# Performance work log

Measured on AMD Instinct MI355X. Metric: run time of the kernel, lower is better.

The kernel has to match this reference:

```python
import jax, jax.numpy as jnp
import numpy as np

B, S, HIDDEN, N_HEADS = 1, 2048, 2048, 16
HEAD_DIM = HIDDEN // N_HEADS  # 128


def setup_inputs() -> dict:
    key = jax.random.key(0)
    ks = jax.random.split(key, 7)
    w = 0.02  # init scale for projection weights
    return {
        "x_self": jax.random.normal(ks[0], (B, S, HIDDEN), jnp.float32),
        "x_cross": jax.random.normal(ks[1], (B, S, HIDDEN), jnp.float32),
        "mask": jnp.zeros((B, 1, S, S), jnp.float32),
        "Wq": jax.random.normal(ks[2], (HIDDEN, HIDDEN), jnp.float32) * w,
        "Wk": jax.random.normal(ks[3], (HIDDEN, HIDDEN), jnp.float32) * w,
        "Wv": jax.random.normal(ks[4], (HIDDEN, HIDDEN), jnp.float32) * w,
        "Wo": jax.random.normal(ks[5], (HIDDEN, HIDDEN), jnp.float32) * w,
    }


def reference(x_self, x_cross, mask, Wq, Wk, Wv, Wo):
    bf16 = jnp.bfloat16
    b = x_self.shape[0]
    scale = HEAD_DIM ** -0.5

    def split_heads(x):  # [b, s, hidden] -> [b, h, s, d]
        return x.reshape(b, -1, N_HEADS, HEAD_DIM).transpose(0, 2, 1, 3)

    # projections run in bf16 (weights cast to bf16 in the original)
    q_self = split_heads((x_self.astype(bf16) @ Wq.astype(bf16).T))
    q_cross = split_heads((x_cross.astype(bf16) @ Wq.astype(bf16).T))
    # k/v for both self and cross blocks come from x_self with identical weights
    k = split_heads((x_self.astype(bf16) @ Wk.astype(bf16).T))
    v = split_heads((x_self.astype(bf16) @ Wv.astype(bf16).T))

    def attn_block(qh):
        # fp32 upcast for QK^T + softmax, then bf16 cast for AV (dropout p=0 -> identity)
        w = jnp.einsum('bhqd,bhkd->bhqk', qh.astype(jnp.float32), k.astype(jnp.float32)) * scale
        w = w + mask
        w = jax.nn.softmax(w, axis=-1).astype(bf16)
        return jnp.einsum('bhqk,bhkd->bhqd', w, v.astype(bf16))  # [b, h, s, d] bf16

    out_self = attn_block(q_self)
    out_cross = attn_block(q_cross)
    out = jnp.concatenate([out_self, out_cross], axis=1)          # [b, 2h, s, d]
    out_flat = out.transpose(0, 2, 1, 3).reshape(b, -1, HIDDEN)   # [b, 2s, hidden]
    Wo_bf = Wo.astype(bf16)
    out_final = 0.5 * (out_flat @ Wo_bf.T + out_flat @ Wo_bf.T)
    return out_final.astype(jnp.float32)
```

## Files before the change

### kernel.cpp

```cpp
#include <hip/hip_runtime.h>
#include <hip/hip_bf16.h>
#include <stdint.h>

#define S 2048
#define HID 2048
#define NH 16
#define HD 128

typedef short short8 __attribute__((ext_vector_type(8)));
typedef float f32x4 __attribute__((ext_vector_type(4)));
typedef float f32x16 __attribute__((ext_vector_type(16)));
typedef uint32_t u32;
typedef u32 u32x4 __attribute__((ext_vector_type(4)));

__device__ __forceinline__ ushort f2bf(float x) {
  uint32_t u = __builtin_bit_cast(uint32_t, x);
  if ((u & 0x7fffffffu) > 0x7f800000u) return (ushort)((u >> 16) | 0x40);
  uint32_t r = u + 0x7fffu + ((u >> 16) & 1u);
  return (ushort)(r >> 16);
}
__device__ __forceinline__ float bf2f(ushort u) {
  union { uint32_t i; float f; } c; c.i = ((uint32_t)u) << 16; return c.f;
}

__device__ __forceinline__ void glds16(const ushort* g, ushort* l) {
  __builtin_amdgcn_global_load_lds((const __attribute__((address_space(1))) uint32_t*)g,
                                   (__attribute__((address_space(3))) uint32_t*)l, 16, 0, 0);
}

__device__ __forceinline__ void mfma16(f32x4& d, short8 a, short8 b) {
  asm volatile("v_mfma_f32_16x16x32_bf16 %0, %1, %2, %0" : "+v"(d) : "v"(a), "v"(b));
}
__device__ __forceinline__ void mfma32(f32x16& d, short8 a, short8 b) {
  asm volatile("v_mfma_f32_32x32x16_bf16 %0, %1, %2, %0" : "+v"(d) : "v"(a), "v"(b));
}
__device__ __forceinline__ f32x16 mfma32_z(short8 a, short8 b) {
  f32x16 d;
  asm volatile("v_mfma_f32_32x32x16_bf16 %0, %1, %2, 0" : "=v"(d) : "v"(a), "v"(b));
  return d;
}
#define MFMA_FENCE() do {                              \
    asm volatile("s_nop 7\n\ts_nop 7\n\ts_nop 7");     \
    __builtin_amdgcn_sched_barrier(0);                 \
  } while (0)
#define RAW_BARRIER() asm volatile("s_barrier" ::: "memory")
#define SCHED_FENCE() __builtin_amdgcn_sched_barrier(0)
#define MAX3(a, b, c) fmaxf(fmaxf((a), (b)), (c))
__device__ __forceinline__ void plswap(u32& a, u32& b) {
  asm volatile("v_permlane32_swap_b32 %0, %1" : "+v"(a), "+v"(b));
}
__device__ __forceinline__ u32 cvtpk(float lo, float hi) {
  u32 r; asm volatile("v_cvt_pk_bf16_f32 %0, %1, %2" : "=v"(r) : "v"(lo), "v"(hi)); return r;
}

struct CastArgs { const float* s[6]; ushort* d[6]; };
__global__ __launch_bounds__(256) void cast6_k(CastArgs a) {
  const float* in = a.s[blockIdx.y];
  ushort* out = a.d[blockIdx.y];
  int i = blockIdx.x * 256 + threadIdx.x;
  float4 v = ((const float4*)in)[i];
  ushort4 o;
  o.x = f2bf(v.x); o.y = f2bf(v.y); o.z = f2bf(v.z); o.w = f2bf(v.w);
  ((ushort4*)out)[i] = o;
}

template <int OUTF32, int NSPLIT>
__device__ __forceinline__ void gemm256_body(const ushort* __restrict__ A,
                                             const ushort* __restrict__ B,
                                             void* __restrict__ C, int N, int K,
                                             long m0, long n0,
                                             ushort* ldsA, ushort* ldsB) {
  const int tid = threadIdx.x, lane = tid & 63, wid = tid >> 6;
  const int g = lane >> 4, c = lane & 15;
  const int wr = wid >> 2, wc = wid & 3;
  const int srow = lane >> 3, sslot = lane & 7;

  f32x4 acc[8][4] = {};

#define GSTAGE256(BO, K0) do {                                                \
    _Pragma("unroll")                                                         \
    for (int i_ = 0; i_ < 4; ++i_) {                                          \
      int ii = wid * 4 + i_;                \
      int rt = ii * 8 + srow;                                                 \
      int col = ((sslot ^ (rt & 7)) << 3) + (K0);                             \
      glds16(A + (m0 + rt) * (long)K + col, ldsA + (BO) * 16384 + ii * 512);  \
      glds16(B + (n0 + rt) * (long)K + col, ldsB + (BO) * 16384 + ii * 512);  \
    } } while (0)

  GSTAGE256(0, 0);

#pragma clang loop unroll(disable)
  for (int k0 = 0; k0 < K; k0 += 64) {
    const int bo = (k0 >> 6) & 1;
    GSTAGE256(bo ^ 1, (k0 + 64 < K) ? (k0 + 64) : 0);
    SCHED_FENCE();
    asm volatile("s_waitcnt vmcnt(8)");
    SCHED_FENCE();
    RAW_BARRIER();
    const ushort* la = ldsA + bo * 16384;
    const ushort* lb = ldsB + bo * 16384;
#pragma unroll
    for (int kk = 0; kk < 2; ++kk) {
      short8 af[8], bfr[4];
#pragma unroll
      for (int m = 0; m < 8; ++m) {
        int row = wr * 128 + m * 16 + c;
        af[m] = *(const short8*)(la + row * 64 + (((kk * 4 + g) ^ (row & 7)) << 3));
      }
#pragma unroll
      for (int n = 0; n < 4; ++n) {
        int row = wc * 64 + n * 16 + c;
        bfr[n] = *(const short8*)(lb + row * 64 + (((kk * 4 + g) ^ (row & 7)) << 3));
      }
#pragma unroll
      for (int m = 0; m < 8; ++m)
#pragma unroll
        for (int n = 0; n < 4; ++n) mfma16(acc[m][n], af[m], bfr[n]);
    }
    RAW_BARRIER();
  }
#undef GSTAGE256
  MFMA_FENCE();
#pragma unroll
  for (int m = 0; m < 8; ++m) {
#pragma unroll
    for (int r = 0; r < 4; ++r) {
      long grow = m0 + wr * 128 + m * 16 + g * 4 + r;
#pragma unroll
      for (int n = 0; n < 4; ++n) {
        long gcol = n0 + wc * 64 + n * 16 + c;
        long idx;
        if (NSPLIT) idx = ((gcol >> 11) << 22) + (grow << 11) + (gcol & 2047);
        else        idx = grow * N + gcol;
        float v = acc[m][n][r];
        if (OUTF32) ((float*)C)[idx] = bf2f(f2bf(v));
        else        ((ushort*)C)[idx] = f2bf(v);
      }
    }
  }
}

__global__ __launch_bounds__(512)
void gemm_qkv256_k(const ushort* __restrict__ xs, const ushort* __restrict__ Wq,
                   ushort* __restrict__ q, const ushort* __restrict__ Wkv,
                   ushort* __restrict__ kv) {
  __shared__ __align__(16) ushort ldsA[2 * 256 * 64];
  __shared__ __align__(16) ushort ldsB[2 * 256 * 64];
  const int bid = blockIdx.x;
  if (bid < 128) {
    gemm256_body<0, 0>(xs, Wq, q, 2048, 2048,
                       (long)(bid >> 3) * 256, (long)(bid & 7) * 256, ldsA, ldsB);
  } else {
    const int b2 = bid - 128;
    gemm256_body<0, 1>(xs, Wkv, kv, 4096, 2048,
                       (long)(b2 >> 4) * 256, (long)(b2 & 15) * 256, ldsA, ldsB);
  }
}

template <int OUTF32, int NSPLIT>
__global__ __launch_bounds__(256)
void gemm_bt_k(const ushort* __restrict__ A, const ushort* __restrict__ B,
               void* __restrict__ C, int M, int N, int K) {
  __shared__ __align__(16) ushort ldsA[128 * 64];
  __shared__ __align__(16) ushort ldsB[128 * 64];
  const int tid = threadIdx.x, lane = tid & 63, wid = tid >> 6;
  const int g = lane >> 4, c = lane & 15;
  const int wr = wid >> 1, wc = wid & 1;
  const long m0 = (long)blockIdx.y * 128, n0 = (long)blockIdx.x * 128;
  const int srow = lane >> 3, sslot = lane & 7;

  f32x4 acc[4][4] = {};

  for (int k0 = 0; k0 < K; k0 += 64) {
#pragma unroll
    for (int i = 0; i < 4; ++i) {
      int ii = wid * 4 + i;
      int rt = ii * 8 + srow;
      int col = ((sslot ^ (rt & 7)) << 3) + k0;
      glds16(A + (m0 + rt) * (long)K + col, ldsA + ii * 512);
      glds16(B + (n0 + rt) * (long)K + col, ldsB + ii * 512);
    }
    __syncthreads();
#pragma unroll
    for (int kk = 0; kk < 2; ++kk) {
      short8 af[4], bfr[4];
#pragma unroll
      for (int m = 0; m < 4; ++m) {
        int row = wr * 64 + m * 16 + c;
        af[m] = *(const short8*)(ldsA + row * 64 + (((kk * 4 + g) ^ (row & 7)) << 3));
      }
#pragma unroll
      for (int n = 0; n < 4; ++n) {
        int row = wc * 64 + n * 16 + c;
        bfr[n] = *(const short8*)(ldsB + row * 64 + (((kk * 4 + g) ^ (row & 7)) << 3));
      }
#pragma unroll
      for (int m = 0; m < 4; ++m)
#pragma unroll
        for (int n = 0; n < 4; ++n) mfma16(acc[m][n], af[m], bfr[n]);
    }
    __syncthreads();
  }
  MFMA_FENCE();
#pragma unroll
  for (int m = 0; m < 4; ++m) {
#pragma unroll
    for (int r = 0; r < 4; ++r) {
      long grow = m0 + wr * 64 + m * 16 + g * 4 + r;
#pragma unroll
      for (int n = 0; n < 4; ++n) {
        long gcol = n0 + wc * 64 + n * 16 + c;
        long idx;
        if (NSPLIT) idx = ((gcol >> 11) << 22) + (grow << 11) + (gcol & 2047);
        else        idx = grow * N + gcol;
        float v = acc[m][n][r];
        if (OUTF32) ((float*)C)[idx] = bf2f(f2bf(v));
        else        ((ushort*)C)[idx] = f2bf(v);
      }
    }
  }
}

__global__ __launch_bounds__(256)
void transpose_bf16_k(const ushort* __restrict__ in, ushort* __restrict__ out) {
  __shared__ __align__(16) ushort t[64][72];
  const int tid = threadIdx.x;
  const long bx = (long)blockIdx.x * 64;
  const long by = (long)blockIdx.y * 64;
#pragma unroll
  for (int i = 0; i < 2; ++i) {
    int row = (tid >> 3) + i * 32;
    int col = (tid & 7) * 8;
    *(short8*)(&t[row][col]) = *(const short8*)(in + (by + row) * 2048 + bx + col);
  }
  __syncthreads();
#pragma unroll
  for (int i = 0; i < 2; ++i) {
    int orow = (tid >> 3) + i * 32;
    int ocol = (tid & 7) * 8;
    short8 v;
#pragma unroll
    for (int j = 0; j < 8; ++j) v[j] = (short)t[ocol + j][orow];
    *(short8*)(out + (bx + orow) * 2048 + by + ocol) = v;
  }
}

__global__ __launch_bounds__(256)
void maskQ_k(const float* __restrict__ in, ushort* __restrict__ out) {
  __shared__ ushort t[64][72];
  const int tid = threadIdx.x;
  const long q0 = (long)blockIdx.y * 64;
  const long k0 = (long)blockIdx.x * 64;
#pragma unroll
  for (int i = 0; i < 4; ++i) {
    int row = i * 16 + (tid >> 4);
    int col = (tid & 15) * 4;
    float4 v = *(const float4*)(in + (q0 + row) * S + k0 + col);
    t[col + 0][row] = f2bf(v.x);
    t[col + 1][row] = f2bf(v.y);
    t[col + 2][row] = f2bf(v.z);
    t[col + 3][row] = f2bf(v.w);
  }
  __syncthreads();
#pragma unroll
  for (int i = 0; i < 4; ++i) {
    int r4 = i * 4 + (tid >> 6);
    int q = tid & 63;
    ushort4 o;
    o.x = t[r4 * 4 + 0][q];
    o.y = t[r4 * 4 + 1][q];
    o.z = t[r4 * 4 + 2][q];
    o.w = t[r4 * 4 + 3][q];
    *(ushort4*)(out + ((k0 >> 2) + r4) * (S * 4) + (q0 + q) * 4) = o;
  }
}

__global__ __launch_bounds__(256)
void attn7_k(const ushort* __restrict__ Qself, const ushort* __restrict__ Qcross,
             const ushort* __restrict__ Kp, const ushort* __restrict__ Vt,
             const ushort* __restrict__ maskQ, ushort* __restrict__ outf) {
  __shared__ __align__(16) ushort ldsK[2 * 64 * 128];
  __shared__ __align__(16) ushort ldsV[2 * 128 * 64];
  const int tid = threadIdx.x, lane = tid & 63, wid = tid >> 6;
  const int c31 = lane & 31, hi = lane >> 5;

  const int b = blockIdx.x;
  const int xcd = b & 7, j = b >> 3;
  const int h = xcd + 8 * (j & 1);
  const int blk = (j >> 1) & 1;
  const int qt = j >> 2;

  const ushort* Qp = blk ? Qcross : Qself;
  const int qbase = qt * 128 + wid * 32;
  const long qme = qbase + c31;

  short8 qf[8];
#pragma unroll
  for (int ks = 0; ks < 8; ++ks)
    qf[ks] = *(const short8*)(Qp + qme * HID + h * HD + ks * 16 + hi * 8);

  f32x16 o[4] = {};
  float m_r = -__builtin_inff(), l_r = 0.f;

  const float SC  = 0.08838834764831845f;
  const float L2E = 1.4426950408889634f;
  const float THR = 5.545177444479562f;

  const int kRow4 = lane >> 4, kSlot = lane & 15;
  const int vRow8 = lane >> 3, vSlot = lane & 7;
  const ushort* mqp = maskQ + qme * 4 + hi * (S * 4);

#define STAGE(BO, KV0) do {                                                       \
    _Pragma("unroll")                                                             \
    for (int i_ = 0; i_ < 4; ++i_) {                                              \
      int seg = i_ * 4 + wid;                                                     \
      int rk = seg * 4 + kRow4;                                                   \
      glds16(Kp + (long)((KV0) + rk) * HID + h * HD + ((kSlot ^ (rk & 15)) << 3), \
             ldsK + (BO) * 8192 + seg * 512);                                     \
      int rv = seg * 8 + vRow8;                                                   \
      glds16(Vt + (long)(h * HD + rv) * S + (KV0) + ((vSlot ^ (rv & 7)) << 3),    \
             ldsV + (BO) * 8192 + seg * 512);                                     \
    }                                                                             \
  } while (0)

  STAGE(0, 0);

#pragma clang loop unroll(disable)
  for (int t = 0; t < 32; ++t) {
    const int bo = t & 1;
    const ushort* kb = ldsK + bo * 8192;
    const ushort* vb = ldsV + bo * 8192;

    ushort4 mq4[8];
#pragma unroll
    for (int jj = 0; jj < 8; ++jj)
      mq4[jj] = *(const ushort4*)(mqp + ((jj & 3) * 2 + (jj >> 2) * 8) * (S * 4));
    SCHED_FENCE();
    STAGE(bo ^ 1, ((t + 1) & 31) * 64);
    SCHED_FENCE();
    asm volatile("s_waitcnt vmcnt(16)");
    SCHED_FENCE();
    RAW_BARRIER();

    f32x16 s0, s1;
    __builtin_amdgcn_s_setprio(1);
    {
      const int r0 = c31, r1 = 32 + c31;
      short8 kf0 = *(const short8*)(kb + r0 * 128 + ((hi ^ (r0 & 15)) << 3));
      short8 kf1 = *(const short8*)(kb + r1 * 128 + ((hi ^ (r1 & 15)) << 3));
      s0 = mfma32_z(kf0, qf[0]);
      s1 = mfma32_z(kf1, qf[0]);
    }
#pragma unroll
    for (int ks = 1; ks < 8; ++ks) {
      int r0 = c31, r1 = 32 + c31;
      short8 kf0 = *(const short8*)(kb + r0 * 128 + (((ks * 2 + hi) ^ (r0 & 15)) << 3));
      short8 kf1 = *(const short8*)(kb + r1 * 128 + (((ks * 2 + hi) ^ (r1 & 15)) << 3));
      mfma32(s0, kf0, qf[ks]);
      mfma32(s1, kf1, qf[ks]);
    }
    __builtin_amdgcn_s_setprio(0);
    MFMA_FENCE();

#pragma unroll
    for (int r = 0; r < 16; ++r) {
      s0[r] = __builtin_fmaf(s0[r], SC, bf2f(mq4[r >> 2][r & 3]));
      s1[r] = __builtin_fmaf(s1[r], SC, bf2f(mq4[4 + (r >> 2)][r & 3]));
    }

    float a0 = MAX3(s0[0], s0[1], s0[2]);
    float a1 = MAX3(s0[3], s0[4], s0[5]);
    float a2 = MAX3(s0[6], s0[7], s0[8]);
    float a3 = MAX3(s0[9], s0[10], s0[11]);
    float a4 = MAX3(s0[12], s0[13], s0[14]);
    float a5 = MAX3(s0[15], s1[0], s1[1]);
    float a6 = MAX3(s1[2], s1[3], s1[4]);
    float a7 = MAX3(s1[5], s1[6], s1[7]);
    float a8 = MAX3(s1[8], s1[9], s1[10]);
    float a9 = MAX3(s1[11], s1[12], s1[13]);
    float a10 = fmaxf(s1[14], s1[15]);
    float b0 = MAX3(a0, a1, a2);
    float b1 = MAX3(a3, a4, a5);
    float b2 = MAX3(a6, a7, a8);
    float b3 = fmaxf(a9, a10);
    float pm = MAX3(b0, b1, fmaxf(b2, b3));
    float pmax = fmaxf(pm, __shfl_xor(pm, 32));

    if (!__all(pmax <= m_r + THR)) {
      float mnew = fmaxf(m_r, pmax);
      float alpha = __builtin_amdgcn_exp2f((m_r - mnew) * L2E);
      m_r = mnew;
      l_r *= alpha;
#pragma unroll
      for (int r = 0; r < 16; ++r) {
        float alf = __shfl(alpha, (r & 3) + 8 * (r >> 2) + 4 * hi);
#pragma unroll
        for (int dt = 0; dt < 4; ++dt) o[dt][r] *= alf;
      }
    }

    const float nm = -m_r * L2E;
#pragma unroll
    for (int r = 0; r < 16; ++r) {
      s0[r] = __builtin_amdgcn_exp2f(__builtin_fmaf(s0[r], L2E, nm));
      s1[r] = __builtin_amdgcn_exp2f(__builtin_fmaf(s1[r], L2E, nm));
    }
    float sm[16];
#pragma unroll
    for (int r = 0; r < 16; ++r) sm[r] = s0[r] + s1[r];
#pragma unroll
    for (int st = 8; st >= 1; st >>= 1)
#pragma unroll
      for (int i = 0; i < 8; ++i)
        if (i < st) sm[i] += sm[i + st];
    l_r += sm[0] + __shfl_xor(sm[0], 32);

    short8 pa[4];
#pragma unroll
    for (int kk = 0; kk < 4; ++kk) {
      const f32x16& sv = (kk < 2) ? s0 : s1;
      const int bq = (kk & 1) * 8;
      u32 x0 = cvtpk(sv[bq + 0], sv[bq + 1]);
      u32 x1 = cvtpk(sv[bq + 2], sv[bq + 3]);
      u32 y0 = cvtpk(sv[bq + 4], sv[bq + 5]);
      u32 y1 = cvtpk(sv[bq + 6], sv[bq + 7]);
      plswap(x0, y0);
      plswap(x1, y1);
      u32x4 tt; tt[0] = x0; tt[1] = x1; tt[2] = y0; tt[3] = y1;
      pa[kk] = __builtin_bit_cast(short8, tt);
    }
    asm volatile("s_nop 1");
    SCHED_FENCE();

    __builtin_amdgcn_s_setprio(1);
#pragma unroll
    for (int kk = 0; kk < 4; ++kk) {
#pragma unroll
      for (int dt = 0; dt < 4; ++dt) {
        int row = dt * 32 + c31;
        short8 vf = *(const short8*)(vb + row * 64 + (((kk * 2 + hi) ^ (row & 7)) << 3));
        mfma32(o[dt], pa[kk], vf);
      }
    }
    __builtin_amdgcn_s_setprio(0);

    RAW_BARRIER();
    mqp += 16 * (S * 4);
  }
#undef STAGE

  MFMA_FENCE();
#pragma unroll
  for (int r = 0; r < 16; ++r) {
    int qr = (r & 3) + 8 * (r >> 2) + 4 * hi;
    float linv = 1.0f / __shfl(l_r, qr);
    long orow = 2L * (qbase + qr) + blk;
#pragma unroll
    for (int dt = 0; dt < 4; ++dt)
      outf[orow * HID + h * HD + dt * 32 + c31] = f2bf(o[dt][r] * linv);
  }
}

extern "C" void kernel_launch(void* const* d_in, const int* in_sizes, int n_in,
                              void* d_out, int out_size, void* d_ws, size_t ws_size,
                              hipStream_t stream) {
  (void)in_sizes; (void)n_in; (void)out_size; (void)ws_size;
  const float* x_self  = (const float*)d_in[0];
  const float* x_cross = (const float*)d_in[1];
  const float* mask    = (const float*)d_in[2];
  const float* Wq      = (const float*)d_in[3];
  const float* Wk      = (const float*)d_in[4];
  const float* Wv      = (const float*)d_in[5];
  const float* Wo      = (const float*)d_in[6];

  uint8_t* w = (uint8_t*)d_ws;
  const size_t MB8 = (size_t)S * HID * sizeof(ushort);
  ushort* xs_bf   = (ushort*)(w + 0 * MB8);
  ushort* xc_bf   = (ushort*)(w + 1 * MB8);
  ushort* Wq_bf   = (ushort*)(w + 2 * MB8);
  ushort* Wk_bf   = (ushort*)(w + 3 * MB8);
  ushort* Wv_bf   = (ushort*)(w + 4 * MB8);
  ushort* Wo_bf   = (ushort*)(w + 5 * MB8);
  ushort* q_self  = (ushort*)(w + 6 * MB8);
  ushort* q_cross = (ushort*)(w + 7 * MB8);
  ushort* k_      = (ushort*)(w + 8 * MB8);
  ushort* v_      = (ushort*)(w + 9 * MB8);
  ushort* vt       = xs_bf;
  ushort* out_flat = Wq_bf;
  ushort* maskQ    = v_;

  CastArgs ca;
  ca.s[0] = x_self;  ca.d[0] = xs_bf;
  ca.s[1] = x_cross; ca.d[1] = xc_bf;
  ca.s[2] = Wq;      ca.d[2] = Wq_bf;
  ca.s[3] = Wk;      ca.d[3] = Wk_bf;
  ca.s[4] = Wv;      ca.d[4] = Wv_bf;
  ca.s[5] = Wo;      ca.d[5] = Wo_bf;
  cast6_k<<<dim3(4096, 6), 256, 0, stream>>>(ca);

  gemm_qkv256_k<<<dim3(256), 512, 0, stream>>>(xs_bf, Wq_bf, q_self, Wk_bf, k_);

  transpose_bf16_k<<<dim3(32, 32), 256, 0, stream>>>(v_, vt);
  maskQ_k<<<dim3(32, 32), 256, 0, stream>>>(mask, maskQ);

  attn7_k<<<dim3(512), 256, 0, stream>>>(q_self, q_cross, k_, vt, maskQ, out_flat);

  gemm_bt_k<1, 0><<<dim3(16, 32), 256, 0, stream>>>(out_flat, Wo_bf, d_out, 4096, 2048, 2048);
}
```

Baseline: 237.1 us.

## Skip mask loads when mask is all zero; double-buffer 256x128 output GEMM

The mask conversion kernel now ORs a device flag when it sees any nonzero mask value. The attention kernel reads that flag and, when the mask is all zero, runs a loop variant that skips the per-tile mask loads and adds, with a tighter vmcnt wait. The output projection GEMM is replaced by a 512-thread, 256x128-tile kernel with double-buffered LDS staging, so global loads overlap the MFMA work. This adds a memset, an atomic and a duplicated loop body, and the flag is stored in the reused x_cross workspace.

New measurement: 236.2 us. About the same (-0.4%).

```diff
diff --git a/kernel.cpp b/kernel.cpp
--- a/kernel.cpp
+++ b/kernel.cpp
@@ -80,7 +80,7 @@
 #define GSTAGE256(BO, K0) do {                                                \
     _Pragma("unroll")                                                         \
     for (int i_ = 0; i_ < 4; ++i_) {                                          \
-      int ii = wid * 4 + i_;                \
+      int ii = wid * 4 + i_;                                                  \
       int rt = ii * 8 + srow;                                                 \
       int col = ((sslot ^ (rt & 7)) << 3) + (K0);                             \
       glds16(A + (m0 + rt) * (long)K + col, ldsA + (BO) * 16384 + ii * 512);  \
@@ -157,50 +157,70 @@
   }
 }
 
-template <int OUTF32, int NSPLIT>
-__global__ __launch_bounds__(256)
-void gemm_bt_k(const ushort* __restrict__ A, const ushort* __restrict__ B,
-               void* __restrict__ C, int M, int N, int K) {
-  __shared__ __align__(16) ushort ldsA[128 * 64];
-  __shared__ __align__(16) ushort ldsB[128 * 64];
+__global__ __launch_bounds__(512)
+void gemm_out256_k(const ushort* __restrict__ A, const ushort* __restrict__ B,
+                   float* __restrict__ C) {
+  __shared__ __align__(16) ushort ldsA[2 * 256 * 64];
+  __shared__ __align__(16) ushort ldsB[2 * 128 * 64];
   const int tid = threadIdx.x, lane = tid & 63, wid = tid >> 6;
   const int g = lane >> 4, c = lane & 15;
   const int wr = wid >> 1, wc = wid & 1;
-  const long m0 = (long)blockIdx.y * 128, n0 = (long)blockIdx.x * 128;
+  const long m0 = (long)(blockIdx.x >> 4) * 256;
+  const long n0 = (long)(blockIdx.x & 15) * 128;
   const int srow = lane >> 3, sslot = lane & 7;
+  const int K = 2048;
 
   f32x4 acc[4][4] = {};
 
+#define OSTAGE(BO, K0) do {                                                   \
+    _Pragma("unroll")                                                         \
+    for (int i_ = 0; i_ < 4; ++i_) {                                          \
+      int ii = wid * 4 + i_;                       \
+      int rt = ii * 8 + srow;                                                 \
+      int col = ((sslot ^ (rt & 7)) << 3) + (K0);                             \
+      glds16(A + (m0 + rt) * (long)K + col, ldsA + (BO) * 16384 + ii * 512);  \
+    }                                                                         \
+    _Pragma("unroll")                                                         \
+    for (int i_ = 0; i_ < 2; ++i_) {                                          \
+      int ii = wid * 2 + i_;                       \
+      int rt = ii * 8 + srow;                                                 \
+      int col = ((sslot ^ (rt & 7)) << 3) + (K0);                             \
+      glds16(B + (n0 + rt) * (long)K + col, ldsB + (BO) * 8192 + ii * 512);   \
+    } } while (0)
+
+  OSTAGE(0, 0);
+
+#pragma clang loop unroll(disable)
   for (int k0 = 0; k0 < K; k0 += 64) {
-#pragma unroll
-    for (int i = 0; i < 4; ++i) {
-      int ii = wid * 4 + i;
-      int rt = ii * 8 + srow;
-      int col = ((sslot ^ (rt & 7)) << 3) + k0;
-      glds16(A + (m0 + rt) * (long)K + col, ldsA + ii * 512);
-      glds16(B + (n0 + rt) * (long)K + col, ldsB + ii * 512);
-    }
-    __syncthreads();
+    const int bo = (k0 >> 6) & 1;
+    OSTAGE(bo ^ 1, (k0 + 64 < K) ? (k0 + 64) : 0);
+    SCHED_FENCE();
+    asm volatile("s_waitcnt vmcnt(6)");
+    SCHED_FENCE();
+    RAW_BARRIER();
+    const ushort* la = ldsA + bo * 16384;
+    const ushort* lb = ldsB + bo * 8192;
 #pragma unroll
     for (int kk = 0; kk < 2; ++kk) {
       short8 af[4], bfr[4];
 #pragma unroll
       for (int m = 0; m < 4; ++m) {
         int row = wr * 64 + m * 16 + c;
-        af[m] = *(const short8*)(ldsA + row * 64 + (((kk * 4 + g) ^ (row & 7)) << 3));
+        af[m] = *(const short8*)(la + row * 64 + (((kk * 4 + g) ^ (row & 7)) << 3));
       }
 #pragma unroll
       for (int n = 0; n < 4; ++n) {
         int row = wc * 64 + n * 16 + c;
-        bfr[n] = *(const short8*)(ldsB + row * 64 + (((kk * 4 + g) ^ (row & 7)) << 3));
+        bfr[n] = *(const short8*)(lb + row * 64 + (((kk * 4 + g) ^ (row & 7)) << 3));
       }
 #pragma unroll
       for (int m = 0; m < 4; ++m)
 #pragma unroll
         for (int n = 0; n < 4; ++n) mfma16(acc[m][n], af[m], bfr[n]);
     }
-    __syncthreads();
-  }
+    RAW_BARRIER();
+  }
+#undef OSTAGE
   MFMA_FENCE();
 #pragma unroll
   for (int m = 0; m < 4; ++m) {
@@ -210,12 +230,7 @@
 #pragma unroll
       for (int n = 0; n < 4; ++n) {
         long gcol = n0 + wc * 64 + n * 16 + c;
-        long idx;
-        if (NSPLIT) idx = ((gcol >> 11) << 22) + (grow << 11) + (gcol & 2047);
-        else        idx = grow * N + gcol;
-        float v = acc[m][n][r];
-        if (OUTF32) ((float*)C)[idx] = bf2f(f2bf(v));
-        else        ((ushort*)C)[idx] = f2bf(v);
+        C[grow * 2048 + gcol] = bf2f(f2bf(acc[m][n][r]));
       }
     }
   }
@@ -246,21 +261,25 @@
 }
 
 __global__ __launch_bounds__(256)
-void maskQ_k(const float* __restrict__ in, ushort* __restrict__ out) {
+void maskQ_k(const float* __restrict__ in, ushort* __restrict__ out,
+             u32* __restrict__ flag) {
   __shared__ ushort t[64][72];
   const int tid = threadIdx.x;
   const long q0 = (long)blockIdx.y * 64;
   const long k0 = (long)blockIdx.x * 64;
+  bool nz = false;
 #pragma unroll
   for (int i = 0; i < 4; ++i) {
     int row = i * 16 + (tid >> 4);
     int col = (tid & 15) * 4;
     float4 v = *(const float4*)(in + (q0 + row) * S + k0 + col);
+    nz = nz || (v.x != 0.f) || (v.y != 0.f) || (v.z != 0.f) || (v.w != 0.f);
     t[col + 0][row] = f2bf(v.x);
     t[col + 1][row] = f2bf(v.y);
     t[col + 2][row] = f2bf(v.z);
     t[col + 3][row] = f2bf(v.w);
   }
+  if (__any(nz) && (tid & 63) == 0) atomicOr(flag, 1u);
   __syncthreads();
 #pragma unroll
   for (int i = 0; i < 4; ++i) {
@@ -278,7 +297,8 @@
 __global__ __launch_bounds__(256)
 void attn7_k(const ushort* __restrict__ Qself, const ushort* __restrict__ Qcross,
              const ushort* __restrict__ Kp, const ushort* __restrict__ Vt,
-             const ushort* __restrict__ maskQ, ushort* __restrict__ outf) {
+             const ushort* __restrict__ maskQ, const u32* __restrict__ flag,
+             ushort* __restrict__ outf) {
   __shared__ __align__(16) ushort ldsK[2 * 64 * 128];
   __shared__ __align__(16) ushort ldsV[2 * 128 * 64];
   const int tid = threadIdx.x, lane = tid & 63, wid = tid >> 6;
@@ -309,6 +329,7 @@
   const int kRow4 = lane >> 4, kSlot = lane & 15;
   const int vRow8 = lane >> 3, vSlot = lane & 7;
   const ushort* mqp = maskQ + qme * 4 + hi * (S * 4);
+  const int nomask = (*flag == 0);
 
 #define STAGE(BO, KV0) do {                                                       \
     _Pragma("unroll")                                                             \
@@ -323,130 +344,136 @@
     }                                                                             \
   } while (0)
 
+#define ABODY(T, WM, VMSTR) do {                                                  \
+    const int bo = (T) & 1;                                                       \
+    const ushort* kb = ldsK + bo * 8192;                                          \
+    const ushort* vb = ldsV + bo * 8192;                                          \
+    ushort4 mq4[8];                                                               \
+    if (WM) {                                                                     \
+      _Pragma("unroll")                                                           \
+      for (int jj = 0; jj < 8; ++jj)                                              \
+        mq4[jj] = *(const ushort4*)(mqp + ((jj & 3) * 2 + (jj >> 2) * 8) * (S * 4)); \
+      SCHED_FENCE();                                                              \
+    }                                                                             \
+    STAGE(bo ^ 1, (((T) + 1) & 31) * 64);                                         \
+    SCHED_FENCE();                                                                \
+    asm volatile(VMSTR);                                                          \
+    SCHED_FENCE();                                                                \
+    RAW_BARRIER();                                                                \
+    f32x16 s0, s1;                                                                \
+    __builtin_amdgcn_s_setprio(1);                                                \
+    {                                                                             \
+      const int r0 = c31, r1 = 32 + c31;                                          \
+      short8 kf0 = *(const short8*)(kb + r0 * 128 + ((hi ^ (r0 & 15)) << 3));     \
+      short8 kf1 = *(const short8*)(kb + r1 * 128 + ((hi ^ (r1 & 15)) << 3));     \
+      s0 = mfma32_z(kf0, qf[0]);                                                  \
+      s1 = mfma32_z(kf1, qf[0]);                                                  \
+    }                                                                             \
+    _Pragma("unroll")                                                             \
+    for (int ks = 1; ks < 8; ++ks) {                                              \
+      int r0 = c31, r1 = 32 + c31;                                                \
+      short8 kf0 = *(const short8*)(kb + r0 * 128 + (((ks * 2 + hi) ^ (r0 & 15)) << 3)); \
+      short8 kf1 = *(const short8*)(kb + r1 * 128 + (((ks * 2 + hi) ^ (r1 & 15)) << 3)); \
+      mfma32(s0, kf0, qf[ks]);                                                    \
+      mfma32(s1, kf1, qf[ks]);                                                    \
+    }                                                                             \
+    __builtin_amdgcn_s_setprio(0);                                                \
+    MFMA_FENCE();                                                                 \
+    if (WM) {                                                                     \
+      _Pragma("unroll")                                                           \
+      for (int r = 0; r < 16; ++r) {                                              \
+        s0[r] = __builtin_fmaf(s0[r], SC, bf2f(mq4[r >> 2][r & 3]));              \
+        s1[r] = __builtin_fmaf(s1[r], SC, bf2f(mq4[4 + (r >> 2)][r & 3]));        \
+      }                                                                           \
+    } else {                                                                      \
+      _Pragma("unroll")                                                           \
+      for (int r = 0; r < 16; ++r) { s0[r] *= SC; s1[r] *= SC; }                  \
+    }                                                                             \
+    float a0 = MAX3(s0[0], s0[1], s0[2]);                                         \
+    float a1 = MAX3(s0[3], s0[4], s0[5]);                                         \
+    float a2 = MAX3(s0[6], s0[7], s0[8]);                                         \
+    float a3 = MAX3(s0[9], s0[10], s0[11]);                                       \
+    float a4 = MAX3(s0[12], s0[13], s0[14]);                                      \
+    float a5 = MAX3(s0[15], s1[0], s1[1]);                                        \
+    float a6 = MAX3(s1[2], s1[3], s1[4]);                                         \
+    float a7 = MAX3(s1[5], s1[6], s1[7]);                                         \
+    float a8 = MAX3(s1[8], s1[9], s1[10]);                                        \
+    float a9 = MAX3(s1[11], s1[12], s1[13]);                                      \
+    float a10 = fmaxf(s1[14], s1[15]);                                            \
+    float b0 = MAX3(a0, a1, a2);                                                  \
+    float b1 = MAX3(a3, a4, a5);                                                  \
+    float b2 = MAX3(a6, a7, a8);                                                  \
+    float b3 = fmaxf(a9, a10);                                                    \
+    float pm = MAX3(b0, b1, fmaxf(b2, b3));                                       \
+    float pmax = fmaxf(pm, __shfl_xor(pm, 32));                                   \
+    if (!__all(pmax <= m_r + THR)) {                                              \
+      float mnew = fmaxf(m_r, pmax);                                              \
+      float alpha = __builtin_amdgcn_exp2f((m_r - mnew) * L2E);                   \
+      m_r = mnew;                                                                 \
+      l_r *= alpha;                                                               \
+      _Pragma("unroll")                                                           \
+      for (int r = 0; r < 16; ++r) {                                              \
+        float alf = __shfl(alpha, (r & 3) + 8 * (r >> 2) + 4 * hi);               \
+        _Pragma("unroll")                                                         \
+        for (int dt = 0; dt < 4; ++dt) o[dt][r] *= alf;                           \
+      }                                                                           \
+    }                                                                             \
+    const float nm = -m_r * L2E;                                                  \
+    _Pragma("unroll")                                                             \
+    for (int r = 0; r < 16; ++r) {                                                \
+      s0[r] = __builtin_amdgcn_exp2f(__builtin_fmaf(s0[r], L2E, nm));             \
+      s1[r] = __builtin_amdgcn_exp2f(__builtin_fmaf(s1[r], L2E, nm));             \
+    }                                                                             \
+    float sm[16];                                                                 \
+    _Pragma("unroll")                                                             \
+    for (int r = 0; r < 16; ++r) sm[r] = s0[r] + s1[r];                           \
+    _Pragma("unroll")                                                             \
+    for (int st = 8; st >= 1; st >>= 1)                                           \
+      _Pragma("unroll")                                                           \
+      for (int i = 0; i < 8; ++i)                                                 \
+        if (i < st) sm[i] += sm[i + st];                                          \
+    l_r += sm[0] + __shfl_xor(sm[0], 32);                                         \
+    short8 pa[4];                                                                 \
+    _Pragma("unroll")                                                             \
+    for (int kk = 0; kk < 4; ++kk) {                                              \
+      const f32x16& sv = (kk < 2) ? s0 : s1;                                      \
+      const int bq = (kk & 1) * 8;                                                \
+      u32 x0 = cvtpk(sv[bq + 0], sv[bq + 1]);                                     \
+      u32 x1 = cvtpk(sv[bq + 2], sv[bq + 3]);                                     \
+      u32 y0 = cvtpk(sv[bq + 4], sv[bq + 5]);                                     \
+      u32 y1 = cvtpk(sv[bq + 6], sv[bq + 7]);                                     \
+      plswap(x0, y0);                                                             \
+      plswap(x1, y1);                                                             \
+      u32x4 tt; tt[0] = x0; tt[1] = x1; tt[2] = y0; tt[3] = y1;                   \
+      pa[kk] = __builtin_bit_cast(short8, tt);                                    \
+    }                                                                             \
+    asm volatile("s_nop 1");                                                      \
+    SCHED_FENCE();                                                                \
+    __builtin_amdgcn_s_setprio(1);                                                \
+    _Pragma("unroll")                                                             \
+    for (int kk = 0; kk < 4; ++kk) {                                              \
+      _Pragma("unroll")                                                           \
+      for (int dt = 0; dt < 4; ++dt) {                                            \
+        int row = dt * 32 + c31;                                                  \
+        short8 vf = *(const short8*)(vb + row * 64 + (((kk * 2 + hi) ^ (row & 7)) << 3)); \
+        mfma32(o[dt], pa[kk], vf);                                                \
+      }                                                                           \
+    }                                                                             \
+    __builtin_amdgcn_s_setprio(0);                                                \
+    RAW_BARRIER();                                                                \
+    if (WM) mqp += 16 * (S * 4);                                                  \
+  } while (0)
+
   STAGE(0, 0);
 
+  if (nomask) {
 #pragma clang loop unroll(disable)
-  for (int t = 0; t < 32; ++t) {
-    const int bo = t & 1;
-    const ushort* kb = ldsK + bo * 8192;
-    const ushort* vb = ldsV + bo * 8192;
-
-    ushort4 mq4[8];
-#pragma unroll
-    for (int jj = 0; jj < 8; ++jj)
-      mq4[jj] = *(const ushort4*)(mqp + ((jj & 3) * 2 + (jj >> 2) * 8) * (S * 4));
-    SCHED_FENCE();
-    STAGE(bo ^ 1, ((t + 1) & 31) * 64);
-    SCHED_FENCE();
-    asm volatile("s_waitcnt vmcnt(16)");
-    SCHED_FENCE();
-    RAW_BARRIER();
-
-    f32x16 s0, s1;
-    __builtin_amdgcn_s_setprio(1);
-    {
-      const int r0 = c31, r1 = 32 + c31;
-      short8 kf0 = *(const short8*)(kb + r0 * 128 + ((hi ^ (r0 & 15)) << 3));
-      short8 kf1 = *(const short8*)(kb + r1 * 128 + ((hi ^ (r1 & 15)) << 3));
-      s0 = mfma32_z(kf0, qf[0]);
-      s1 = mfma32_z(kf1, qf[0]);
-    }
-#pragma unroll
-    for (int ks = 1; ks < 8; ++ks) {
-      int r0 = c31, r1 = 32 + c31;
-      short8 kf0 = *(const short8*)(kb + r0 * 128 + (((ks * 2 + hi) ^ (r0 & 15)) << 3));
-      short8 kf1 = *(const short8*)(kb + r1 * 128 + (((ks * 2 + hi) ^ (r1 & 15)) << 3));
-      mfma32(s0, kf0, qf[ks]);
-      mfma32(s1, kf1, qf[ks]);
-    }
-    __builtin_amdgcn_s_setprio(0);
-    MFMA_FENCE();
-
-#pragma unroll
-    for (int r = 0; r < 16; ++r) {
-      s0[r] = __builtin_fmaf(s0[r], SC, bf2f(mq4[r >> 2][r & 3]));
-      s1[r] = __builtin_fmaf(s1[r], SC, bf2f(mq4[4 + (r >> 2)][r & 3]));
-    }
-
-    float a0 = MAX3(s0[0], s0[1], s0[2]);
-    float a1 = MAX3(s0[3], s0[4], s0[5]);
-    float a2 = MAX3(s0[6], s0[7], s0[8]);
-    float a3 = MAX3(s0[9], s0[10], s0[11]);
-    float a4 = MAX3(s0[12], s0[13], s0[14]);
-    float a5 = MAX3(s0[15], s1[0], s1[1]);
-    float a6 = MAX3(s1[2], s1[3], s1[4]);
-    float a7 = MAX3(s1[5], s1[6], s1[7]);
-    float a8 = MAX3(s1[8], s1[9], s1[10]);
-    float a9 = MAX3(s1[11], s1[12], s1[13]);
-    float a10 = fmaxf(s1[14], s1[15]);
-    float b0 = MAX3(a0, a1, a2);
-    float b1 = MAX3(a3, a4, a5);
-    float b2 = MAX3(a6, a7, a8);
-    float b3 = fmaxf(a9, a10);
-    float pm = MAX3(b0, b1, fmaxf(b2, b3));
-    float pmax = fmaxf(pm, __shfl_xor(pm, 32));
-
-    if (!__all(pmax <= m_r + THR)) {
-      float mnew = fmaxf(m_r, pmax);
-      float alpha = __builtin_amdgcn_exp2f((m_r - mnew) * L2E);
-      m_r = mnew;
-      l_r *= alpha;
-#pragma unroll
-      for (int r = 0; r < 16; ++r) {
-        float alf = __shfl(alpha, (r & 3) + 8 * (r >> 2) + 4 * hi);
-#pragma unroll
-        for (int dt = 0; dt < 4; ++dt) o[dt][r] *= alf;
-      }
-    }
-
-    const float nm = -m_r * L2E;
-#pragma unroll
-    for (int r = 0; r < 16; ++r) {
-      s0[r] = __builtin_amdgcn_exp2f(__builtin_fmaf(s0[r], L2E, nm));
-      s1[r] = __builtin_amdgcn_exp2f(__builtin_fmaf(s1[r], L2E, nm));
-    }
-    float sm[16];
-#pragma unroll
-    for (int r = 0; r < 16; ++r) sm[r] = s0[r] + s1[r];
-#pragma unroll
-    for (int st = 8; st >= 1; st >>= 1)
-#pragma unroll
-      for (int i = 0; i < 8; ++i)
-        if (i < st) sm[i] += sm[i + st];
-    l_r += sm[0] + __shfl_xor(sm[0], 32);
-
-    short8 pa[4];
-#pragma unroll
-    for (int kk = 0; kk < 4; ++kk) {
-      const f32x16& sv = (kk < 2) ? s0 : s1;
-      const int bq = (kk & 1) * 8;
-      u32 x0 = cvtpk(sv[bq + 0], sv[bq + 1]);
-      u32 x1 = cvtpk(sv[bq + 2], sv[bq + 3]);
-      u32 y0 = cvtpk(sv[bq + 4], sv[bq + 5]);
-      u32 y1 = cvtpk(sv[bq + 6], sv[bq + 7]);
-      plswap(x0, y0);
-      plswap(x1, y1);
-      u32x4 tt; tt[0] = x0; tt[1] = x1; tt[2] = y0; tt[3] = y1;
-      pa[kk] = __builtin_bit_cast(short8, tt);
-    }
-    asm volatile("s_nop 1");
-    SCHED_FENCE();
-
-    __builtin_amdgcn_s_setprio(1);
-#pragma unroll
-    for (int kk = 0; kk < 4; ++kk) {
-#pragma unroll
-      for (int dt = 0; dt < 4; ++dt) {
-        int row = dt * 32 + c31;
-        short8 vf = *(const short8*)(vb + row * 64 + (((kk * 2 + hi) ^ (row & 7)) << 3));
-        mfma32(o[dt], pa[kk], vf);
-      }
-    }
-    __builtin_amdgcn_s_setprio(0);
-
-    RAW_BARRIER();
-    mqp += 16 * (S * 4);
-  }
+    for (int t = 0; t < 32; ++t) { ABODY(t, 0, "s_waitcnt vmcnt(8)"); }
+  } else {
+#pragma clang loop unroll(disable)
+    for (int t = 0; t < 32; ++t) { ABODY(t, 1, "s_waitcnt vmcnt(16)"); }
+  }
+#undef ABODY
 #undef STAGE
 
   MFMA_FENCE();
@@ -488,6 +515,7 @@
   ushort* vt       = xs_bf;
   ushort* out_flat = Wq_bf;
   ushort* maskQ    = v_;
+  u32*    mflag    = (u32*)xc_bf;
 
   CastArgs ca;
   ca.s[0] = x_self;  ca.d[0] = xs_bf;
@@ -501,9 +529,10 @@
   gemm_qkv256_k<<<dim3(256), 512, 0, stream>>>(xs_bf, Wq_bf, q_self, Wk_bf, k_);
 
   transpose_bf16_k<<<dim3(32, 32), 256, 0, stream>>>(v_, vt);
-  maskQ_k<<<dim3(32, 32), 256, 0, stream>>>(mask, maskQ);
-
-  attn7_k<<<dim3(512), 256, 0, stream>>>(q_self, q_cross, k_, vt, maskQ, out_flat);
-
-  gemm_bt_k<1, 0><<<dim3(16, 32), 256, 0, stream>>>(out_flat, Wo_bf, d_out, 4096, 2048, 2048);
-}
+  hipMemsetAsync(mflag, 0, 4, stream);
+  maskQ_k<<<dim3(32, 32), 256, 0, stream>>>(mask, maskQ, mflag);
+
+  attn7_k<<<dim3(512), 256, 0, stream>>>(q_self, q_cross, k_, vt, maskQ, mflag, out_flat);
+
+  gemm_out256_k<<<dim3(256), 512, 0, stream>>>(out_flat, Wo_bf, (float*)d_out);
+}
```
